# Optimization experiments

Measured on AMD Instinct MI355X. Metric: run time of the kernel, lower is better.

The kernel has to match this reference:

```python
import jax, jax.numpy as jnp
import numpy as np

N_FEATURES = 512
K = 4
BATCH = 1024

# static upper-triangle pair indices (j1 < j2)
_I1, _I2 = np.triu_indices(N_FEATURES, k=1)
I1 = jnp.asarray(_I1)
I2 = jnp.asarray(_I2)


def setup_inputs() -> dict:
    key = jax.random.key(0)
    kx, kw = jax.random.split(key)
    x = jax.random.normal(kx, (BATCH, N_FEATURES), dtype=jnp.float32)
    # RandomNormal initializer default stddev=0.05
    weight = jax.random.normal(kw, (N_FEATURES, K), dtype=jnp.float32) * 0.05
    return {"x": x, "weight": weight}


def reference(x, weight):
    # per-pair latent dot products: <w_{j1}, w_{j2}> for all j1 < j2  -> [P]
    wdot = jnp.einsum("pk,pk->p", weight[I1], weight[I2])
    # out[b, p] = wdot[p] * x[b, j1(p)] * x[b, j2(p)]  -> [B, P]
    return x[:, I1] * x[:, I2] * wdot[None, :]
```

## Files before the change

kernel.cpp:

```cpp
#include <hip/hip_runtime.h>


#define NF      512
#define KDIM    4
#define BATCH   1024
#define NPAIRS  130816
#define WDPAD   131072
#define CHUNK   4096
#define NCHUNK  32
#define TPB     256
#define BT      16

__device__ __forceinline__ int rowoff(int j) {
    return (j * (1023 - j)) >> 1;
}

__global__ __launch_bounds__(TPB) void fm_wdot(
    const float* __restrict__ w,
    float* __restrict__ wd)
{
    const int j1 = blockIdx.x;
    if (j1 == NF - 1) {
        wd[NPAIRS + threadIdx.x] = 0.f;
        return;
    }
    const int L   = (NF - 1) - j1;
    const int off = rowoff(j1);
    const float wa0 = w[j1*KDIM+0], wa1 = w[j1*KDIM+1],
                wa2 = w[j1*KDIM+2], wa3 = w[j1*KDIM+3];
    for (int t = threadIdx.x; t < L; t += TPB) {
        const int j2 = j1 + 1 + t;
        wd[off + t] = wa0*w[j2*KDIM+0] + wa1*w[j2*KDIM+1]
                    + wa2*w[j2*KDIM+2] + wa3*w[j2*KDIM+3];
    }
}

__global__ __launch_bounds__(TPB) void fm_main(
    const float* __restrict__ x,
    const float* __restrict__ wd,
    float* __restrict__ out)
{
    __shared__ float xs[NF];
    __shared__ float wbuf[2][CHUNK];

    const int b = blockIdx.x;
    const int t = threadIdx.x;

    {
        if (t < NF/4)
            reinterpret_cast<float4*>(xs)[t] =
                reinterpret_cast<const float4*>(x + (size_t)b * NF)[t];
        const float4* s0 = reinterpret_cast<const float4*>(wd);
        float4* d0 = reinterpret_cast<float4*>(wbuf[0]);
#pragma unroll
        for (int i = 0; i < 4; ++i) d0[t + TPB*i] = s0[t + TPB*i];
    }
    __syncthreads();

    float* const obase = out + (size_t)b * NPAIRS;

    for (int c = 0; c < NCHUNK; ++c) {
        float4 st0, st1, st2, st3;
        if (c + 1 < NCHUNK) {
            const float4* s = reinterpret_cast<const float4*>(wd + (c + 1) * CHUNK);
            st0 = s[t];          st1 = s[t + TPB];
            st2 = s[t + 2*TPB];  st3 = s[t + 3*TPB];
        }

        const float* wb = wbuf[c & 1];
        const int p0 = c * CHUNK;
        const int klim = (NPAIRS - p0 >= CHUNK) ? (CHUNK / TPB)
                                                : ((NPAIRS - p0) / TPB);
        for (int k = 0; k < klim; ++k) {
            const int pl = (k << 8) + t;
            const int p  = p0 + pl;
            const float s = sqrtf((float)(1046529 - 8 * p));
            int j1 = (int)((1023.0f - s) * 0.5f);
            j1 = j1 < 0 ? 0 : (j1 > 510 ? 510 : j1);
            while (rowoff(j1 + 1) <= p) ++j1;
            while (rowoff(j1) > p) --j1;
            const int j2 = p - rowoff(j1) + j1 + 1;
            obase[p] = wb[pl] * xs[j1] * xs[j2];
        }

        if (c + 1 < NCHUNK) {
            float4* d = reinterpret_cast<float4*>(wbuf[(c + 1) & 1]);
            d[t] = st0; d[t + TPB] = st1; d[t + 2*TPB] = st2; d[t + 3*TPB] = st3;
        }
        __syncthreads();
    }
}

__global__ __launch_bounds__(TPB) void fm_kernel(
    const float* __restrict__ x,
    const float* __restrict__ w,
    float* __restrict__ out)
{
    const int j1  = blockIdx.x;
    const int b0  = blockIdx.y * BT;
    const int L   = (NF - 1) - j1;
    const int off = j1 * (NF - 1) - (j1 * (j1 - 1)) / 2;

    const float wa0 = w[j1 * KDIM + 0];
    const float wa1 = w[j1 * KDIM + 1];
    const float wa2 = w[j1 * KDIM + 2];
    const float wa3 = w[j1 * KDIM + 3];

    __shared__ float wdl[NF - 1];
    for (int t = threadIdx.x; t < L; t += TPB) {
        const int j2 = j1 + 1 + t;
        wdl[t] = wa0 * w[j2 * KDIM + 0] + wa1 * w[j2 * KDIM + 1]
               + wa2 * w[j2 * KDIM + 2] + wa3 * w[j2 * KDIM + 3];
    }
    __syncthreads();

    for (int bi = 0; bi < BT; ++bi) {
        const int b = b0 + bi;
        const float xj1 = x[(size_t)b * NF + j1];
        const float* __restrict__ xrow = x + (size_t)b * NF + (j1 + 1);
        float* __restrict__ orow = out + (size_t)b * NPAIRS + off;
        for (int t = threadIdx.x; t < L; t += TPB) {
            orow[t] = wdl[t] * xj1 * xrow[t];
        }
    }
}

extern "C" void kernel_launch(void* const* d_in, const int* in_sizes, int n_in,
                              void* d_out, int out_size, void* d_ws, size_t ws_size,
                              hipStream_t stream) {
    const float* x = (const float*)d_in[0];
    const float* w = (const float*)d_in[1];
    float* out = (float*)d_out;

    if (ws_size >= (size_t)WDPAD * sizeof(float)) {
        float* wd = (float*)d_ws;
        fm_wdot<<<dim3(NF), TPB, 0, stream>>>(w, wd);
        fm_main<<<dim3(BATCH), TPB, 0, stream>>>(x, wd, out);
    } else {
        dim3 grid(NF - 1, BATCH / BT);
        fm_kernel<<<grid, TPB, 0, stream>>>(x, w, out);
    }
}
```

Baseline: 617.8 us.

## Vectorize FM output stores with float4 nontemporal writes and split pairs across blocks

```diff
diff --git a/kernel.cpp b/kernel.cpp
--- a/kernel.cpp
+++ b/kernel.cpp
@@ -6,10 +6,13 @@
 #define BATCH   1024
 #define NPAIRS  130816
 #define WDPAD   131072
-#define CHUNK   4096
-#define NCHUNK  32
 #define TPB     256
+#define SPLIT   2
+#define PBLK    (WDPAD / SPLIT)
+#define NIT     (PBLK / (TPB * 4))
 #define BT      16
+
+typedef float f32x4 __attribute__((ext_vector_type(4)));
 
 __device__ __forceinline__ int rowoff(int j) {
     return (j * (1023 - j)) >> 1;
@@ -35,59 +38,55 @@
     }
 }
 
-__global__ __launch_bounds__(TPB) void fm_main(
+__global__ __launch_bounds__(TPB) void fm_main2(
     const float* __restrict__ x,
     const float* __restrict__ wd,
     float* __restrict__ out)
 {
     __shared__ float xs[NF];
-    __shared__ float wbuf[2][CHUNK];
 
     const int b = blockIdx.x;
     const int t = threadIdx.x;
 
-    {
-        if (t < NF/4)
-            reinterpret_cast<float4*>(xs)[t] =
-                reinterpret_cast<const float4*>(x + (size_t)b * NF)[t];
-        const float4* s0 = reinterpret_cast<const float4*>(wd);
-        float4* d0 = reinterpret_cast<float4*>(wbuf[0]);
-#pragma unroll
-        for (int i = 0; i < 4; ++i) d0[t + TPB*i] = s0[t + TPB*i];
-    }
+    if (t < NF / 4)
+        reinterpret_cast<f32x4*>(xs)[t] =
+            reinterpret_cast<const f32x4*>(x + (size_t)b * NF)[t];
     __syncthreads();
 
+    const int pbase = blockIdx.y * PBLK;
     float* const obase = out + (size_t)b * NPAIRS;
 
-    for (int c = 0; c < NCHUNK; ++c) {
-        float4 st0, st1, st2, st3;
-        if (c + 1 < NCHUNK) {
-            const float4* s = reinterpret_cast<const float4*>(wd + (c + 1) * CHUNK);
-            st0 = s[t];          st1 = s[t + TPB];
-            st2 = s[t + 2*TPB];  st3 = s[t + 3*TPB];
-        }
+    f32x4 wv = *reinterpret_cast<const f32x4*>(wd + pbase + (t << 2));
 
-        const float* wb = wbuf[c & 1];
-        const int p0 = c * CHUNK;
-        const int klim = (NPAIRS - p0 >= CHUNK) ? (CHUNK / TPB)
-                                                : ((NPAIRS - p0) / TPB);
-        for (int k = 0; k < klim; ++k) {
-            const int pl = (k << 8) + t;
-            const int p  = p0 + pl;
+    for (int it = 0; it < NIT; ++it) {
+        const int p = pbase + it * (TPB * 4) + (t << 2);
+
+        f32x4 nwv = (f32x4){0.f, 0.f, 0.f, 0.f};
+        if (it + 1 < NIT)
+            nwv = *reinterpret_cast<const f32x4*>(wd + p + TPB * 4);
+
+        if (p < NPAIRS) {
             const float s = sqrtf((float)(1046529 - 8 * p));
             int j1 = (int)((1023.0f - s) * 0.5f);
             j1 = j1 < 0 ? 0 : (j1 > 510 ? 510 : j1);
-            while (rowoff(j1 + 1) <= p) ++j1;
-            while (rowoff(j1) > p) --j1;
-            const int j2 = p - rowoff(j1) + j1 + 1;
-            obase[p] = wb[pl] * xs[j1] * xs[j2];
+            int len = 511 - j1;
+            int r   = (j1 * (1023 - j1)) >> 1;
+            while (r > p)        { --j1; ++len; r -= len; }
+            while (p >= r + len) { r += len; --len; ++j1; }
+
+            float xj1 = xs[j1];
+            f32x4 o;
+            o.x = wv.x * xj1 * xs[p     - r + j1 + 1];
+            if (p + 1 >= r + len) { r += len; --len; ++j1; xj1 = xs[j1]; }
+            o.y = wv.y * xj1 * xs[p + 1 - r + j1 + 1];
+            if (p + 2 >= r + len) { r += len; --len; ++j1; xj1 = xs[j1]; }
+            o.z = wv.z * xj1 * xs[p + 2 - r + j1 + 1];
+            if (p + 3 >= r + len) { r += len; --len; ++j1; xj1 = xs[j1]; }
+            o.w = wv.w * xj1 * xs[p + 3 - r + j1 + 1];
+
+            __builtin_nontemporal_store(o, reinterpret_cast<f32x4*>(obase + p));
         }
-
-        if (c + 1 < NCHUNK) {
-            float4* d = reinterpret_cast<float4*>(wbuf[(c + 1) & 1]);
-            d[t] = st0; d[t + TPB] = st1; d[t + 2*TPB] = st2; d[t + 3*TPB] = st3;
-        }
-        __syncthreads();
+        wv = nwv;
     }
 }
 
@@ -135,7 +134,7 @@
     if (ws_size >= (size_t)WDPAD * sizeof(float)) {
         float* wd = (float*)d_ws;
         fm_wdot<<<dim3(NF), TPB, 0, stream>>>(w, wd);
-        fm_main<<<dim3(BATCH), TPB, 0, stream>>>(x, wd, out);
+        fm_main2<<<dim3(BATCH, SPLIT), TPB, 0, stream>>>(x, wd, out);
     } else {
         dim3 grid(NF - 1, BATCH / BT);
         fm_kernel<<<grid, TPB, 0, stream>>>(x, w, out);
```

New measurement: 532.9 us. 1.16x faster.
